# Kernel optimization log

Hardware: AMD Instinct MI355X
Metric: run time of the kernel (lower is better)

## Reference

```python
import jax, jax.numpy as jnp
import numpy as np

B, IN_DIM, H, OUT_DIM, T = 2048, 1024, 2048, 1024, 10


def setup_inputs() -> dict:
    key = jax.random.key(0)
    ks = jax.random.split(key, 16)
    s = lambda d: 1.0 / np.sqrt(d)
    inp = {
        "x": jax.random.normal(ks[0], (B, IN_DIM), jnp.float32),
        "z0": jax.random.normal(ks[1], (B, H), jnp.float32),
        "noise": jax.random.normal(ks[2], (T, B, H), jnp.float32),
        # input_embed: Linear(IN,H) -> SiLU -> Linear(H,H)
        "w1_in": jax.random.normal(ks[3], (IN_DIM, H), jnp.float32) * s(IN_DIM),
        "b1_in": jnp.zeros((H,), jnp.float32),
        "w2_in": jax.random.normal(ks[4], (H, H), jnp.float32) * s(H),
        "b2_in": jnp.zeros((H,), jnp.float32),
        # T blocks: Linear(2H,H) -> SiLU -> Linear(H,H), stacked over T
        "wA": jax.random.normal(ks[5], (T, 2 * H, H), jnp.float32) * s(2 * H),
        "bA": jnp.zeros((T, H), jnp.float32),
        "wB": jax.random.normal(ks[6], (T, H, H), jnp.float32) * s(H),
        "bB": jnp.zeros((T, H), jnp.float32),
        # classifier Linear(H, OUT)
        "wC": jax.random.normal(ks[7], (H, OUT_DIM), jnp.float32) * s(H),
        "bC": jnp.zeros((OUT_DIM,), jnp.float32),
    }
    return inp


def _forward(x, z0, noise, w1_in, b1_in, w2_in, b2_in, wA, bA, wB, bB, wC, bC):
    # input embedding
    h = jax.nn.silu(x @ w1_in + b1_in)
    x_embed = h @ w2_in + b2_in  # (B, H)

    alpha = jnp.linspace(0.99, 0.9, T).astype(x.dtype)          # (T,)
    noise_scale = jnp.sqrt(1.0 - alpha)                          # (T,)

    def step(z, per_t):
        wA_t, bA_t, wB_t, bB_t, n_t, a_t, ns_t = per_t
        u = jax.nn.silu(jnp.concatenate([z, x_embed], axis=-1) @ wA_t + bA_t)
        u = u @ wB_t + bB_t
        z_next = a_t * u + (1.0 - a_t) * z + ns_t * n_t
        return z_next, None

    z_final, _ = jax.lax.scan(step, z0, (wA, bA, wB, bB, noise, alpha, noise_scale))
    return z_final @ wC + bC  # (B, OUT_DIM)


def reference(x, z0, noise, w1_in, b1_in, w2_in, b2_in, wA, bA, wB, bB, wC, bC):
    return _forward(x, z0, noise, w1_in, b1_in, w2_in, b2_in, wA, bA, wB, bB, wC, bC)
```

## Files before the change

### kernel.cpp

```cpp
#include <hip/hip_runtime.h>
#include <math.h>

typedef _Float16 f16;
typedef _Float16 f16x4 __attribute__((ext_vector_type(4)));
typedef _Float16 f16x8 __attribute__((ext_vector_type(8)));
typedef float f32x4 __attribute__((ext_vector_type(4)));
typedef float fvec4 __attribute__((ext_vector_type(4)));

#define EP_SILU 0
#define EP_LIN  1
#define EP_ZUP  2
#define EP_OUT  3
#define EP_ADDP 4

struct TDesc {
  const float* W;
  f16* WT;
  long long sW, sWT;
  int R, C, nMat;
};

__device__ __forceinline__ void gll16(const void* g, void* l) {
  __builtin_amdgcn_global_load_lds((__attribute__((address_space(1))) void*)g,
                                   (__attribute__((address_space(3))) void*)l,
                                   16, 0, 0);
}

__device__ __forceinline__ void stage_tile(const f16* __restrict__ g, int ld,
                                           f16* ldsTile, int tid, int wid) {
#pragma unroll
  for (int p = 0; p < 2; ++p) {
    int row = p * 64 + (tid >> 2);
    int col = (tid & 3) * 8;
    gll16(g + (size_t)row * ld + col, ldsTile + p * 2048 + wid * 512);
  }
}

__device__ __forceinline__ void stage8s(const f16* __restrict__ g, int ld,
                                        f16* ldsTile, int tid) {
  int row = tid >> 2;
  int q = (tid & 3) ^ ((tid >> 3) & 3);
  gll16(g + (size_t)row * ld + q * 8, ldsTile + tid * 8);
}

__device__ __forceinline__ void tpose_tile(const float* __restrict__ W,
                                           f16* __restrict__ WT, int R, int C,
                                           int r0, int c0, f16 (*t)[72],
                                           int tid) {
#pragma unroll
  for (int p = 0; p < 2; ++p) {
    int lin = p * 2048 + tid * 4;
    int r = lin >> 6, c4 = lin & 63;
    fvec4 v = *(const fvec4*)(W + (size_t)(r0 + r) * C + c0 + c4);
    t[c4 + 0][r] = (f16)v[0];
    t[c4 + 1][r] = (f16)v[1];
    t[c4 + 2][r] = (f16)v[2];
    t[c4 + 3][r] = (f16)v[3];
  }
  __syncthreads();
#pragma unroll
  for (int p = 0; p < 2; ++p) {
    int lin = p * 2048 + tid * 4;
    int c = lin >> 6, r4 = lin & 63;
    f16x4 h;
    h[0] = t[c][r4 + 0];
    h[1] = t[c][r4 + 1];
    h[2] = t[c][r4 + 2];
    h[3] = t[c][r4 + 3];
    *(f16x4*)(WT + (size_t)(c0 + c) * R + r0 + r4) = h;
  }
  __syncthreads();
}

__device__ void run_role(const TDesc d, int rid, int nr, f16 (*t)[72],
                         int tid) {
  if (d.nMat <= 0 || d.W == nullptr) return;
  int tR = d.R >> 6, tC = d.C >> 6;
  int tpm = tR * tC, tot = tpm * d.nMat;
  for (int i = rid; i < tot; i += nr) {
    int m = i / tpm, rem = i - m * tpm;
    int r0 = (rem % tR) << 6, c0 = (rem / tR) << 6;
    tpose_tile(d.W + (size_t)m * d.sW, d.WT + (size_t)m * d.sWT, d.R, d.C, r0,
               c0, t, tid);
  }
}

#define GEMM8_ITER(KP, VM, DO_STAGE)                                          \
  {                                                                           \
    asm volatile("s_waitcnt vmcnt(" #VM ")" ::: "memory");                    \
    __builtin_amdgcn_s_barrier();                                             \
    const int slot_ = (KP) & 1;                                               \
    const f16* LA_ = base + slot_ * 16384 + h * 4096;                         \
    const f16* LB_ = base + slot_ * 16384 + 8192 + h * 4096;                  \
    f16x8 a_[4], b_[4];                                                       \
    _Pragma("unroll") for (int m_ = 0; m_ < 4; ++m_) a_[m_] =                 \
        *(const f16x8*)(LA_ +                                                 \
                        ((wr * 64 + m_ * 16 + lr) * 32 + (kg ^ xq) * 8));     \
    _Pragma("unroll") for (int n_ = 0; n_ < 4; ++n_) b_[n_] =                 \
        *(const f16x8*)(LB_ +                                                 \
                        ((wc * 64 + n_ * 16 + lr) * 32 + (kg ^ xq) * 8));     \
    asm volatile("s_waitcnt lgkmcnt(0)" ::: "memory");                        \
    __builtin_amdgcn_s_barrier();                                             \
    if (DO_STAGE) stageAB((KP) + 2, slot_);                                   \
    _Pragma("unroll") for (int m_ = 0; m_ < 4; ++m_)                          \
        _Pragma("unroll") for (int n_ = 0; n_ < 4; ++n_) acc[m_][n_] =        \
            __builtin_amdgcn_mfma_f32_16x16x32_f16(a_[m_], b_[n_],            \
                                                   acc[m_][n_], 0, 0, 0);     \
  }

template <int EP>
__global__ void __launch_bounds__(512)
gemm8(const f16* __restrict__ A, int lda, const f16* __restrict__ BT, int ldb,
      long long sBT, int K, int N, int gx, int nbGemm,
      const float* __restrict__ bias, long long sBias,
      const f16* __restrict__ addP, f16* __restrict__ outH,
      float* __restrict__ outF, long long sOut, const f16* __restrict__ zOld,
      const float* __restrict__ noise, float aT, float nsT, TDesc dA,
      TDesc dB) {
  __shared__ __align__(16) char smem[65536];
  const int tid = threadIdx.x;
  const int bid = blockIdx.x;

  if (bid >= nbGemm) {
    if (blockIdx.z == 0) {
      int rid = bid - nbGemm, nr = (int)gridDim.x - nbGemm;
      f16(*t)[72] = reinterpret_cast<f16(*)[72]>(smem);
      run_role(dA, rid, nr, t, tid);
      run_role(dB, rid, nr, t, tid);
    }
    return;
  }

  const int z = blockIdx.z;
  const f16* BTz = BT + (size_t)z * sBT;
  f16* outHz = outH ? outH + (size_t)z * sOut : nullptr;
  float* outFz = outF ? outF + (size_t)z * sOut : nullptr;

  const int cpx = nbGemm >> 3;
  const int swz = (bid & 7) * cpx + (bid >> 3);
  const int by = swz / gx, bx = swz % gx;
  const int m0 = by * 128, n0 = bx * 128;

  const int lane = tid & 63, wid = tid >> 6;
  const int q = wid & 3, h = wid >> 2;
  const int wr = q >> 1, wc = q & 1;
  const int lr = lane & 15, kg = lane >> 4;
  const int xq = (lr >> 1) & 3;

  f16* base = (f16*)smem;
  f32x4 acc[4][4] = {};

  const int nkp = K >> 6;
  auto stageAB = [&](int kp, int slot) {
    int k0 = kp << 6;
    f16* s = base + slot * 16384;
    stage8s(A + (size_t)m0 * lda + k0, lda, s, tid);
    stage8s(A + (size_t)m0 * lda + k0 + 32, lda, s + 4096, tid);
    stage8s(BTz + (size_t)n0 * ldb + k0, ldb, s + 8192, tid);
    stage8s(BTz + (size_t)n0 * ldb + k0 + 32, ldb, s + 12288, tid);
  };

  stageAB(0, 0);
  stageAB(1, 1);
  int kp = 0;
  for (; kp < nkp - 1; ++kp) GEMM8_ITER(kp, 4, (kp + 2 < nkp));
  GEMM8_ITER(kp, 0, 0);

  float* red = (float*)smem;
  if (h == 1) {
#pragma unroll
    for (int m = 0; m < 4; ++m)
#pragma unroll
      for (int n = 0; n < 4; ++n) {
        int row = wr * 64 + m * 16 + kg * 4;
        int col = wc * 64 + n * 16 + lr;
        int rs = row ^ ((col & 7) << 2);
        *(f32x4*)&red[(size_t)col * 128 + rs] = acc[m][n];
      }
  }
  __syncthreads();
  if (h != 0) return;

  float bcol[4];
  if constexpr (EP != EP_ADDP) {
    const float* biasz = bias + (size_t)z * sBias;
#pragma unroll
    for (int n = 0; n < 4; ++n) bcol[n] = biasz[n0 + wc * 64 + n * 16 + lr];
  }

#pragma unroll
  for (int m = 0; m < 4; ++m) {
    int rowb = m0 + wr * 64 + m * 16 + kg * 4;
    int rowl = wr * 64 + m * 16 + kg * 4;
#pragma unroll
    for (int n = 0; n < 4; ++n) {
      int col = n0 + wc * 64 + n * 16 + lr;
      int coll = wc * 64 + n * 16 + lr;
      int rsl = rowl ^ ((coll & 7) << 2);
      f32x4 osum = acc[m][n] + *(const f32x4*)&red[(size_t)coll * 128 + rsl];
#pragma unroll
      for (int r = 0; r < 4; ++r) {
        size_t idx = (size_t)(rowb + r) * N + col;
        float v = osum[r];
        if constexpr (EP == EP_ADDP) v += (float)addP[idx];
        else v += bcol[n];
        if constexpr (EP == EP_SILU || EP == EP_ADDP) {
          v = v / (1.0f + __expf(-v));
          outHz[idx] = (f16)v;
        } else if constexpr (EP == EP_LIN) {
          outHz[idx] = (f16)v;
        } else if constexpr (EP == EP_OUT) {
          outFz[idx] = v;
        } else {
          float zn = aT * v + (1.0f - aT) * (float)zOld[idx] + nsT * noise[idx];
          outHz[idx] = (f16)zn;
        }
      }
    }
  }
}

template <int EP>
__global__ void __launch_bounds__(256)
gemm_bt(const f16* __restrict__ A0, const f16* __restrict__ A1, int Ksplit,
        int lda, const f16* __restrict__ BT, int ldb, long long sBT, int K,
        int N, int gx, const float* __restrict__ bias, long long sBias,
        f16* __restrict__ outH, float* __restrict__ outF, long long sOut,
        const float* __restrict__ zOld, const float* __restrict__ noise,
        float aT, float nsT) {
  __shared__ __align__(16) f16 lds[2][2][128 * 32];
  const int tid = threadIdx.x;
  const int z = blockIdx.z;
  const f16* BTz = BT + (size_t)z * sBT;
  f16* outHz = outH ? outH + (size_t)z * sOut : nullptr;
  float* outFz = outF ? outF + (size_t)z * sOut : nullptr;

  const int lane = tid & 63, wid = tid >> 6;
  const int wr = wid >> 1, wc = wid & 1;
  const int lr = lane & 15, kg = lane >> 4;
  const int by = blockIdx.x / gx, bx = blockIdx.x - by * gx;
  const int m0 = by * 128, n0 = bx * 128;

  f32x4 acc[4][4] = {};
  const int nk = K >> 5;
  auto stageAB = [&](int kt, int buf) {
    int k0 = kt << 5;
    const f16* Abase = (k0 < Ksplit)
                           ? (A0 + (size_t)m0 * lda + k0)
                           : (A1 + (size_t)m0 * lda + (k0 - Ksplit));
    stage_tile(Abase, lda, &lds[buf][0][0], tid, wid);
    stage_tile(BTz + (size_t)n0 * ldb + k0, ldb, &lds[buf][1][0], tid, wid);
  };

  stageAB(0, 0);
  __syncthreads();
  int cur = 0;
  for (int kt = 0; kt < nk; ++kt) {
    if (kt + 1 < nk) stageAB(kt + 1, cur ^ 1);
    const f16* LA = &lds[cur][0][0];
    const f16* LB = &lds[cur][1][0];
    f16x8 a[4], b[4];
#pragma unroll
    for (int m = 0; m < 4; ++m)
      a[m] = *(const f16x8*)(LA + ((wr * 64 + m * 16 + lr) * 32 + kg * 8));
#pragma unroll
    for (int n = 0; n < 4; ++n)
      b[n] = *(const f16x8*)(LB + ((wc * 64 + n * 16 + lr) * 32 + kg * 8));
#pragma unroll
    for (int m = 0; m < 4; ++m)
#pragma unroll
      for (int n = 0; n < 4; ++n)
        acc[m][n] = __builtin_amdgcn_mfma_f32_16x16x32_f16(a[m], b[n],
                                                           acc[m][n], 0, 0, 0);
    __syncthreads();
    cur ^= 1;
  }

  float bcol[4];
  const float* biasz = bias + (size_t)z * sBias;
#pragma unroll
  for (int n = 0; n < 4; ++n) bcol[n] = biasz[n0 + wc * 64 + n * 16 + lr];

#pragma unroll
  for (int m = 0; m < 4; ++m) {
    int rowb = m0 + wr * 64 + m * 16 + kg * 4;
#pragma unroll
    for (int n = 0; n < 4; ++n) {
      int col = n0 + wc * 64 + n * 16 + lr;
#pragma unroll
      for (int r = 0; r < 4; ++r) {
        size_t idx = (size_t)(rowb + r) * N + col;
        float v = acc[m][n][r] + bcol[n];
        if constexpr (EP == EP_SILU) {
          v = v / (1.0f + __expf(-v));
          outHz[idx] = (f16)v;
        } else if constexpr (EP == EP_LIN) {
          outHz[idx] = (f16)v;
        } else if constexpr (EP == EP_OUT) {
          outFz[idx] = v;
        } else {
          float zn = aT * v + (1.0f - aT) * zOld[idx] + nsT * noise[idx];
          outFz[idx] = zn;
          outHz[idx] = (f16)zn;
        }
      }
    }
  }
}

__global__ void __launch_bounds__(512) tconv_role(TDesc d) {
  __shared__ __align__(16) f16 t[64][72];
  run_role(d, blockIdx.x, gridDim.x, t, threadIdx.x);
}

__global__ void __launch_bounds__(256)
cvt4(const float* __restrict__ in, f16* __restrict__ outp, int n4) {
  int i = blockIdx.x * 256 + threadIdx.x;
  if (i >= n4) return;
  fvec4 v = *(const fvec4*)(in + (size_t)i * 4);
  f16x4 h;
  h[0] = (f16)v[0];
  h[1] = (f16)v[1];
  h[2] = (f16)v[2];
  h[3] = (f16)v[3];
  *(f16x4*)(outp + (size_t)i * 4) = h;
}

__global__ void __launch_bounds__(256)
zinit4(const float* __restrict__ z0, float* __restrict__ z32,
       f16* __restrict__ z16, int n4) {
  int i = blockIdx.x * 256 + threadIdx.x;
  if (i >= n4) return;
  fvec4 v = *(const fvec4*)(z0 + (size_t)i * 4);
  *(fvec4*)(z32 + (size_t)i * 4) = v;
  f16x4 h;
  h[0] = (f16)v[0];
  h[1] = (f16)v[1];
  h[2] = (f16)v[2];
  h[3] = (f16)v[3];
  *(f16x4*)(z16 + (size_t)i * 4) = h;
}

extern "C" void kernel_launch(void* const* d_in, const int* in_sizes, int n_in,
                              void* d_out, int out_size, void* d_ws,
                              size_t ws_size, hipStream_t stream) {
  const int B = 2048, IN = 1024, H = 2048, OUT = 1024, T = 10;
  const float* x = (const float*)d_in[0];
  const float* z0 = (const float*)d_in[1];
  const float* noise = (const float*)d_in[2];
  const float* w1 = (const float*)d_in[3];
  const float* b1 = (const float*)d_in[4];
  const float* w2 = (const float*)d_in[5];
  const float* b2 = (const float*)d_in[6];
  const float* wA = (const float*)d_in[7];
  const float* bA = (const float*)d_in[8];
  const float* wB = (const float*)d_in[9];
  const float* bB = (const float*)d_in[10];
  const float* wC = (const float*)d_in[11];
  const float* bC = (const float*)d_in[12];
  float* out = (float*)d_out;

  char* ws = (char*)d_ws;
  size_t off = 0;
  auto alloc = [&](size_t bytes) {
    void* p = ws + off;
    off += (bytes + 255) & ~(size_t)255;
    return p;
  };
  TDesc none = {nullptr, nullptr, 0, 0, 0, 0, 0};

  const size_t FAST_NEED = 273000000ull;
  if (ws_size >= FAST_NEED) {
    f16* x16 = (f16*)alloc((size_t)B * IN * 2);
    f16* h16 = (f16*)alloc((size_t)B * H * 2);
    f16* xe16 = (f16*)alloc((size_t)B * H * 2);
    f16* z16 = (f16*)alloc((size_t)B * H * 2);
    f16* u16 = (f16*)alloc((size_t)B * H * 2);
    f16* p16 = (f16*)alloc((size_t)T * B * H * 2);
    f16* w1T = (f16*)alloc((size_t)IN * H * 2);
    f16* w2T = (f16*)alloc((size_t)H * H * 2);
    f16* wCT = (f16*)alloc((size_t)H * OUT * 2);
    f16* wAbotT = (f16*)alloc((size_t)T * H * H * 2);
    f16* wAtopT[2] = {(f16*)alloc((size_t)H * H * 2),
                      (f16*)alloc((size_t)H * H * 2)};
    f16* wBT2[2] = {(f16*)alloc((size_t)H * H * 2),
                    (f16*)alloc((size_t)H * H * 2)};

    cvt4<<<B * IN / 4 / 256, 256, 0, stream>>>(x, x16, B * IN / 4);
    cvt4<<<B * H / 4 / 256, 256, 0, stream>>>(z0, z16, B * H / 4);
    tconv_role<<<512, 512, 0, stream>>>(TDesc{w1, w1T, 0, 0, IN, H, 1});

    gemm8<EP_SILU><<<512, 512, 0, stream>>>(
        x16, IN, w1T, IN, 0, IN, H, 16, 256, b1, 0, nullptr, h16, nullptr, 0,
        nullptr, nullptr, 0.f, 0.f, TDesc{w2, w2T, 0, 0, H, H, 1},
        TDesc{wA + (size_t)H * H, wAbotT, (long long)2 * H * H,
              (long long)H * H, H, H, 4});
    gemm8<EP_LIN><<<512, 512, 0, stream>>>(
        h16, H, w2T, H, 0, H, H, 16, 256, b2, 0, nullptr, xe16, nullptr, 0,
        nullptr, nullptr, 0.f, 0.f, TDesc{wC, wCT, 0, 0, H, OUT, 1},
        TDesc{wA + (size_t)H * H + (size_t)4 * 2 * H * H,
              wAbotT + (size_t)4 * H * H, (long long)2 * H * H,
              (long long)H * H, H, H, 6});
    tconv_role<<<512, 512, 0, stream>>>(TDesc{wA, wAtopT[0], 0, 0, H, H, 1});

    gemm8<EP_LIN><<<dim3(256, 1, T), 512, 0, stream>>>(
        xe16, H, wAbotT, H, (long long)H * H, H, H, 16, 256, bA, H, nullptr,
        p16, nullptr, (long long)B * H, nullptr, nullptr, 0.f, 0.f, none,
        none);

    for (int t = 0; t < T; ++t) {
      float alpha = (float)(0.99 - 0.01 * (double)t);
      float ns = sqrtf(1.0f - alpha);
      gemm8<EP_ADDP><<<320, 512, 0, stream>>>(
          z16, H, wAtopT[t & 1], H, 0, H, H, 16, 256, nullptr, 0,
          p16 + (size_t)t * B * H, u16, nullptr, 0, nullptr, nullptr, 0.f,
          0.f, TDesc{wB + (size_t)t * H * H, wBT2[t & 1], 0, 0, H, H, 1},
          none);
      TDesc nextA = (t < T - 1)
                        ? TDesc{wA + (size_t)(t + 1) * 2 * H * H,
                                wAtopT[(t + 1) & 1], 0, 0, H, H, 1}
                        : none;
      gemm8<EP_ZUP><<<320, 512, 0, stream>>>(
          u16, H, wBT2[t & 1], H, 0, H, H, 16, 256, bB + (size_t)t * H, 0,
          nullptr, z16, nullptr, 0, z16, noise + (size_t)t * B * H, alpha, ns,
          nextA, none);
    }
    gemm8<EP_OUT><<<128, 512, 0, stream>>>(
        z16, H, wCT, H, 0, H, OUT, 8, 128, bC, 0, nullptr, nullptr, out, 0,
        nullptr, nullptr, 0.f, 0.f, none, none);
  } else {
    f16* x16 = (f16*)alloc((size_t)B * IN * 2);
    f16* h16 = (f16*)alloc((size_t)B * H * 2);
    f16* xe16 = (f16*)alloc((size_t)B * H * 2);
    f16* z16 = (f16*)alloc((size_t)B * H * 2);
    f16* u16 = (f16*)alloc((size_t)B * H * 2);
    float* z32 = (float*)alloc((size_t)B * H * 4);
    f16* w1T = (f16*)alloc((size_t)IN * H * 2);
    f16* w2T = (f16*)alloc((size_t)H * H * 2);
    f16* wCT = (f16*)alloc((size_t)H * OUT * 2);
    f16* wAT = (f16*)alloc((size_t)2 * H * H * 2);
    f16* wBT = (f16*)alloc((size_t)H * H * 2);

    cvt4<<<B * IN / 4 / 256, 256, 0, stream>>>(x, x16, B * IN / 4);
    zinit4<<<B * H / 4 / 256, 256, 0, stream>>>(z0, z32, z16, B * H / 4);
    tconv_role<<<512, 512, 0, stream>>>(TDesc{w1, w1T, 0, 0, IN, H, 1});
    tconv_role<<<1024, 512, 0, stream>>>(TDesc{w2, w2T, 0, 0, H, H, 1});
    tconv_role<<<512, 512, 0, stream>>>(TDesc{wC, wCT, 0, 0, H, OUT, 1});

    gemm_bt<EP_SILU><<<dim3(256, 1, 1), 256, 0, stream>>>(
        x16, x16, IN, IN, w1T, IN, 0, IN, H, 16, b1, 0, h16, nullptr, 0,
        nullptr, nullptr, 0.f, 0.f);
    gemm_bt<EP_LIN><<<dim3(256, 1, 1), 256, 0, stream>>>(
        h16, h16, H, H, w2T, H, 0, H, H, 16, b2, 0, xe16, nullptr, 0, nullptr,
        nullptr, 0.f, 0.f);

    for (int t = 0; t < T; ++t) {
      float alpha = (float)(0.99 - 0.01 * (double)t);
      float ns = sqrtf(1.0f - alpha);
      tconv_role<<<1024, 512, 0, stream>>>(
          TDesc{wA + (size_t)t * 2 * H * H, wAT, 0, 0, 2 * H, H, 1});
      gemm_bt<EP_SILU><<<dim3(256, 1, 1), 256, 0, stream>>>(
          z16, xe16, H, H, wAT, 2 * H, 0, 2 * H, H, 16, bA + (size_t)t * H, 0,
          u16, nullptr, 0, nullptr, nullptr, 0.f, 0.f);
      tconv_role<<<1024, 512, 0, stream>>>(
          TDesc{wB + (size_t)t * H * H, wBT, 0, 0, H, H, 1});
      gemm_bt<EP_ZUP><<<dim3(256, 1, 1), 256, 0, stream>>>(
          u16, u16, H, H, wBT, H, 0, H, H, 16, bB + (size_t)t * H, 0, z16,
          z32, 0, z32, noise + (size_t)t * B * H, alpha, ns);
    }
    gemm_bt<EP_OUT><<<dim3(128, 1, 1), 256, 0, stream>>>(
        z16, z16, H, H, wCT, H, 0, H, OUT, 8, bC, 0, nullptr, out, 0, nullptr,
        nullptr, 0.f, 0.f);
  }
}
```

Baseline: 1.109 ms.

## Fuse recurrent timestep loop into one persistent kernel with per-panel barriers

Replaces the 20 per-timestep GEMM launches and the final classifier launch with one persistent 256-block kernel. Each group of 16 blocks owns one 128-row panel of z and syncs through atomic-counter barriers instead of kernel boundaries. All wA-top and wB transposes now run up front, as extra blocks of the batched p-projection GEMM. This removes launch gaps and tail effects, at the cost of more workspace, spin-wait barriers and a dependence on all 256 blocks being resident at once.

```diff
diff --git a/kernel.cpp b/kernel.cpp
--- a/kernel.cpp
+++ b/kernel.cpp
@@ -109,18 +109,98 @@
   }
 
 template <int EP>
+__device__ __forceinline__ void
+gphase(const f16* __restrict__ A, int lda, const f16* __restrict__ BT,
+       int ldb, int K, int N, int m0, int n0, const float* __restrict__ bias,
+       const f16* __restrict__ addP, f16* __restrict__ outH,
+       float* __restrict__ outF, const f16* __restrict__ zOld,
+       const float* __restrict__ noise, float aT, float nsT, f16* base,
+       int tid) {
+  const int lane = tid & 63, wid = tid >> 6;
+  const int q = wid & 3, h = wid >> 2;
+  const int wr = q >> 1, wc = q & 1;
+  const int lr = lane & 15, kg = lane >> 4;
+  const int xq = (lr >> 1) & 3;
+
+  f32x4 acc[4][4] = {};
+  const int nkp = K >> 6;
+  auto stageAB = [&](int kp, int slot) {
+    int k0 = kp << 6;
+    f16* s = base + slot * 16384;
+    stage8s(A + (size_t)m0 * lda + k0, lda, s, tid);
+    stage8s(A + (size_t)m0 * lda + k0 + 32, lda, s + 4096, tid);
+    stage8s(BT + (size_t)n0 * ldb + k0, ldb, s + 8192, tid);
+    stage8s(BT + (size_t)n0 * ldb + k0 + 32, ldb, s + 12288, tid);
+  };
+
+  stageAB(0, 0);
+  stageAB(1, 1);
+  int kp = 0;
+  for (; kp < nkp - 1; ++kp) GEMM8_ITER(kp, 4, (kp + 2 < nkp));
+  GEMM8_ITER(kp, 0, 0);
+
+  float* red = (float*)base;
+  if (h == 1) {
+#pragma unroll
+    for (int m = 0; m < 4; ++m)
+#pragma unroll
+      for (int n = 0; n < 4; ++n) {
+        int row = wr * 64 + m * 16 + kg * 4;
+        int col = wc * 64 + n * 16 + lr;
+        int rs = row ^ ((col & 7) << 2);
+        *(f32x4*)&red[(size_t)col * 128 + rs] = acc[m][n];
+      }
+  }
+  __syncthreads();
+  if (h == 0) {
+    float bcol[4];
+    if constexpr (EP != EP_ADDP) {
+#pragma unroll
+      for (int n = 0; n < 4; ++n) bcol[n] = bias[n0 + wc * 64 + n * 16 + lr];
+    }
+#pragma unroll
+    for (int m = 0; m < 4; ++m) {
+      int rowb = m0 + wr * 64 + m * 16 + kg * 4;
+      int rowl = wr * 64 + m * 16 + kg * 4;
+#pragma unroll
+      for (int n = 0; n < 4; ++n) {
+        int col = n0 + wc * 64 + n * 16 + lr;
+        int coll = wc * 64 + n * 16 + lr;
+        int rsl = rowl ^ ((coll & 7) << 2);
+        f32x4 osum =
+            acc[m][n] + *(const f32x4*)&red[(size_t)coll * 128 + rsl];
+#pragma unroll
+        for (int r = 0; r < 4; ++r) {
+          size_t idx = (size_t)(rowb + r) * N + col;
+          float v = osum[r];
+          if constexpr (EP == EP_ADDP) v += (float)addP[idx];
+          else v += bcol[n];
+          if constexpr (EP == EP_SILU || EP == EP_ADDP) {
+            v = v / (1.0f + __expf(-v));
+            outH[idx] = (f16)v;
+          } else if constexpr (EP == EP_LIN) {
+            outH[idx] = (f16)v;
+          } else if constexpr (EP == EP_OUT) {
+            outF[idx] = v;
+          } else {
+            float zn =
+                aT * v + (1.0f - aT) * (float)zOld[idx] + nsT * noise[idx];
+            outH[idx] = (f16)zn;
+          }
+        }
+      }
+    }
+  }
+}
+
+template <int EP>
 __global__ void __launch_bounds__(512)
 gemm8(const f16* __restrict__ A, int lda, const f16* __restrict__ BT, int ldb,
       long long sBT, int K, int N, int gx, int nbGemm,
-      const float* __restrict__ bias, long long sBias,
-      const f16* __restrict__ addP, f16* __restrict__ outH,
-      float* __restrict__ outF, long long sOut, const f16* __restrict__ zOld,
-      const float* __restrict__ noise, float aT, float nsT, TDesc dA,
-      TDesc dB) {
+      const float* __restrict__ bias, long long sBias, f16* __restrict__ outH,
+      long long sOut, TDesc dA, TDesc dB) {
   __shared__ __align__(16) char smem[65536];
-  const int tid = threadIdx.x;
-  const int bid = blockIdx.x;
-
+  const int tid = threadIdx.x, bid = blockIdx.x;
   if (bid >= nbGemm) {
     if (blockIdx.z == 0) {
       int rid = bid - nbGemm, nr = (int)gridDim.x - nbGemm;
@@ -130,94 +210,62 @@
     }
     return;
   }
-
   const int z = blockIdx.z;
-  const f16* BTz = BT + (size_t)z * sBT;
-  f16* outHz = outH ? outH + (size_t)z * sOut : nullptr;
-  float* outFz = outF ? outF + (size_t)z * sOut : nullptr;
-
   const int cpx = nbGemm >> 3;
   const int swz = (bid & 7) * cpx + (bid >> 3);
   const int by = swz / gx, bx = swz % gx;
-  const int m0 = by * 128, n0 = bx * 128;
-
-  const int lane = tid & 63, wid = tid >> 6;
-  const int q = wid & 3, h = wid >> 2;
-  const int wr = q >> 1, wc = q & 1;
-  const int lr = lane & 15, kg = lane >> 4;
-  const int xq = (lr >> 1) & 3;
-
+  gphase<EP>(A, lda, BT + (size_t)z * sBT, ldb, K, N, by * 128, bx * 128,
+             bias + (size_t)z * sBias, nullptr, outH + (size_t)z * sOut,
+             nullptr, nullptr, nullptr, 0.f, 0.f, (f16*)smem, tid);
+}
+
+__device__ __forceinline__ void panelbar(unsigned* cnt, unsigned target,
+                                         int tid) {
+  __syncthreads();
+  if (tid == 0) {
+    __threadfence();
+    atomicAdd(cnt, 1u);
+    while (atomicAdd(cnt, 0u) < target) __builtin_amdgcn_s_sleep(2);
+    __threadfence();
+  }
+  __syncthreads();
+}
+
+__global__ void __launch_bounds__(512)
+fused_loop(f16* __restrict__ z16, f16* __restrict__ u16,
+           const f16* __restrict__ p16, const f16* __restrict__ wAtopT,
+           const f16* __restrict__ wBT, const float* __restrict__ bB,
+           const float* __restrict__ noise, const f16* __restrict__ wCT,
+           const float* __restrict__ bC, float* __restrict__ out,
+           unsigned* __restrict__ bar) {
+  constexpr int H = 2048, Bv = 2048, T = 10, OUTD = 1024;
+  __shared__ __align__(16) char smem[65536];
   f16* base = (f16*)smem;
-  f32x4 acc[4][4] = {};
-
-  const int nkp = K >> 6;
-  auto stageAB = [&](int kp, int slot) {
-    int k0 = kp << 6;
-    f16* s = base + slot * 16384;
-    stage8s(A + (size_t)m0 * lda + k0, lda, s, tid);
-    stage8s(A + (size_t)m0 * lda + k0 + 32, lda, s + 4096, tid);
-    stage8s(BTz + (size_t)n0 * ldb + k0, ldb, s + 8192, tid);
-    stage8s(BTz + (size_t)n0 * ldb + k0 + 32, ldb, s + 12288, tid);
-  };
-
-  stageAB(0, 0);
-  stageAB(1, 1);
-  int kp = 0;
-  for (; kp < nkp - 1; ++kp) GEMM8_ITER(kp, 4, (kp + 2 < nkp));
-  GEMM8_ITER(kp, 0, 0);
-
-  float* red = (float*)smem;
-  if (h == 1) {
-#pragma unroll
-    for (int m = 0; m < 4; ++m)
-#pragma unroll
-      for (int n = 0; n < 4; ++n) {
-        int row = wr * 64 + m * 16 + kg * 4;
-        int col = wc * 64 + n * 16 + lr;
-        int rs = row ^ ((col & 7) << 2);
-        *(f32x4*)&red[(size_t)col * 128 + rs] = acc[m][n];
-      }
-  }
-  __syncthreads();
-  if (h != 0) return;
-
-  float bcol[4];
-  if constexpr (EP != EP_ADDP) {
-    const float* biasz = bias + (size_t)z * sBias;
-#pragma unroll
-    for (int n = 0; n < 4; ++n) bcol[n] = biasz[n0 + wc * 64 + n * 16 + lr];
-  }
-
-#pragma unroll
-  for (int m = 0; m < 4; ++m) {
-    int rowb = m0 + wr * 64 + m * 16 + kg * 4;
-    int rowl = wr * 64 + m * 16 + kg * 4;
-#pragma unroll
-    for (int n = 0; n < 4; ++n) {
-      int col = n0 + wc * 64 + n * 16 + lr;
-      int coll = wc * 64 + n * 16 + lr;
-      int rsl = rowl ^ ((coll & 7) << 2);
-      f32x4 osum = acc[m][n] + *(const f32x4*)&red[(size_t)coll * 128 + rsl];
-#pragma unroll
-      for (int r = 0; r < 4; ++r) {
-        size_t idx = (size_t)(rowb + r) * N + col;
-        float v = osum[r];
-        if constexpr (EP == EP_ADDP) v += (float)addP[idx];
-        else v += bcol[n];
-        if constexpr (EP == EP_SILU || EP == EP_ADDP) {
-          v = v / (1.0f + __expf(-v));
-          outHz[idx] = (f16)v;
-        } else if constexpr (EP == EP_LIN) {
-          outHz[idx] = (f16)v;
-        } else if constexpr (EP == EP_OUT) {
-          outFz[idx] = v;
-        } else {
-          float zn = aT * v + (1.0f - aT) * (float)zOld[idx] + nsT * noise[idx];
-          outHz[idx] = (f16)zn;
-        }
-      }
-    }
-  }
+  const int tid = threadIdx.x, bid = blockIdx.x;
+  const int s = bid >> 3;
+  const int ch = (bid & 7) + 8 * (s >> 4);
+  const int bx = s & 15;
+  const int m0 = ch * 128;
+  unsigned gen = 0;
+  unsigned* cnt = bar + ch * 32;
+
+  for (int t = 0; t < T; ++t) {
+    float alpha = (float)(0.99 - 0.01 * (double)t);
+    float ns = sqrtf(1.0f - alpha);
+    gphase<EP_ADDP>(z16, H, wAtopT + (size_t)t * H * H, H, H, H, m0, bx * 128,
+                    nullptr, p16 + (size_t)t * Bv * H, u16, nullptr, nullptr,
+                    nullptr, 0.f, 0.f, base, tid);
+    ++gen;
+    panelbar(cnt, 16u * gen, tid);
+    gphase<EP_ZUP>(u16, H, wBT + (size_t)t * H * H, H, H, H, m0, bx * 128,
+                   bB + (size_t)t * H, nullptr, z16, nullptr, z16,
+                   noise + (size_t)t * Bv * H, alpha, ns, base, tid);
+    ++gen;
+    panelbar(cnt, 16u * gen, tid);
+  }
+  if (bx < 8)
+    gphase<EP_OUT>(z16, H, wCT, H, H, OUTD, m0, bx * 128, bC, nullptr,
+                   nullptr, out, nullptr, nullptr, 0.f, 0.f, base, tid);
 }
 
 template <int EP>
@@ -369,8 +417,9 @@
   };
   TDesc none = {nullptr, nullptr, 0, 0, 0, 0, 0};
 
-  const size_t FAST_NEED = 273000000ull;
+  const size_t FAST_NEED = 380000000ull;
   if (ws_size >= FAST_NEED) {
+    unsigned* bar = (unsigned*)alloc(2048);
     f16* x16 = (f16*)alloc((size_t)B * IN * 2);
     f16* h16 = (f16*)alloc((size_t)B * H * 2);
     f16* xe16 = (f16*)alloc((size_t)B * H * 2);
@@ -381,53 +430,34 @@
     f16* w2T = (f16*)alloc((size_t)H * H * 2);
     f16* wCT = (f16*)alloc((size_t)H * OUT * 2);
     f16* wAbotT = (f16*)alloc((size_t)T * H * H * 2);
-    f16* wAtopT[2] = {(f16*)alloc((size_t)H * H * 2),
-                      (f16*)alloc((size_t)H * H * 2)};
-    f16* wBT2[2] = {(f16*)alloc((size_t)H * H * 2),
-                    (f16*)alloc((size_t)H * H * 2)};
-
+    f16* wAtopT = (f16*)alloc((size_t)T * H * H * 2);
+    f16* wBTall = (f16*)alloc((size_t)T * H * H * 2);
+
+    hipMemsetAsync(bar, 0, 2048, stream);
     cvt4<<<B * IN / 4 / 256, 256, 0, stream>>>(x, x16, B * IN / 4);
     cvt4<<<B * H / 4 / 256, 256, 0, stream>>>(z0, z16, B * H / 4);
     tconv_role<<<512, 512, 0, stream>>>(TDesc{w1, w1T, 0, 0, IN, H, 1});
 
     gemm8<EP_SILU><<<512, 512, 0, stream>>>(
-        x16, IN, w1T, IN, 0, IN, H, 16, 256, b1, 0, nullptr, h16, nullptr, 0,
-        nullptr, nullptr, 0.f, 0.f, TDesc{w2, w2T, 0, 0, H, H, 1},
+        x16, IN, w1T, IN, 0, IN, H, 16, 256, b1, 0, h16, 0,
+        TDesc{w2, w2T, 0, 0, H, H, 1},
         TDesc{wA + (size_t)H * H, wAbotT, (long long)2 * H * H,
-              (long long)H * H, H, H, 4});
+              (long long)H * H, H, H, 5});
     gemm8<EP_LIN><<<512, 512, 0, stream>>>(
-        h16, H, w2T, H, 0, H, H, 16, 256, b2, 0, nullptr, xe16, nullptr, 0,
-        nullptr, nullptr, 0.f, 0.f, TDesc{wC, wCT, 0, 0, H, OUT, 1},
-        TDesc{wA + (size_t)H * H + (size_t)4 * 2 * H * H,
-              wAbotT + (size_t)4 * H * H, (long long)2 * H * H,
-              (long long)H * H, H, H, 6});
-    tconv_role<<<512, 512, 0, stream>>>(TDesc{wA, wAtopT[0], 0, 0, H, H, 1});
-
-    gemm8<EP_LIN><<<dim3(256, 1, T), 512, 0, stream>>>(
-        xe16, H, wAbotT, H, (long long)H * H, H, H, 16, 256, bA, H, nullptr,
-        p16, nullptr, (long long)B * H, nullptr, nullptr, 0.f, 0.f, none,
-        none);
-
-    for (int t = 0; t < T; ++t) {
-      float alpha = (float)(0.99 - 0.01 * (double)t);
-      float ns = sqrtf(1.0f - alpha);
-      gemm8<EP_ADDP><<<320, 512, 0, stream>>>(
-          z16, H, wAtopT[t & 1], H, 0, H, H, 16, 256, nullptr, 0,
-          p16 + (size_t)t * B * H, u16, nullptr, 0, nullptr, nullptr, 0.f,
-          0.f, TDesc{wB + (size_t)t * H * H, wBT2[t & 1], 0, 0, H, H, 1},
-          none);
-      TDesc nextA = (t < T - 1)
-                        ? TDesc{wA + (size_t)(t + 1) * 2 * H * H,
-                                wAtopT[(t + 1) & 1], 0, 0, H, H, 1}
-                        : none;
-      gemm8<EP_ZUP><<<320, 512, 0, stream>>>(
-          u16, H, wBT2[t & 1], H, 0, H, H, 16, 256, bB + (size_t)t * H, 0,
-          nullptr, z16, nullptr, 0, z16, noise + (size_t)t * B * H, alpha, ns,
-          nextA, none);
-    }
-    gemm8<EP_OUT><<<128, 512, 0, stream>>>(
-        z16, H, wCT, H, 0, H, OUT, 8, 128, bC, 0, nullptr, nullptr, out, 0,
-        nullptr, nullptr, 0.f, 0.f, none, none);
+        h16, H, w2T, H, 0, H, H, 16, 256, b2, 0, xe16, 0,
+        TDesc{wC, wCT, 0, 0, H, OUT, 1},
+        TDesc{wA + (size_t)H * H + (size_t)5 * 2 * H * H,
+              wAbotT + (size_t)5 * H * H, (long long)2 * H * H,
+              (long long)H * H, H, H, 5});
+
+    gemm8<EP_LIN><<<dim3(384, 1, T), 512, 0, stream>>>(
+        xe16, H, wAbotT, H, (long long)H * H, H, H, 16, 256, bA, H, p16,
+        (long long)B * H,
+        TDesc{wA, wAtopT, (long long)2 * H * H, (long long)H * H, H, H, 10},
+        TDesc{wB, wBTall, (long long)H * H, (long long)H * H, H, H, 10});
+
+    fused_loop<<<256, 512, 0, stream>>>(z16, u16, p16, wAtopT, wBTall, bB,
+                                        noise, wCT, bC, out, bar);
   } else {
     f16* x16 = (f16*)alloc((size_t)B * IN * 2);
     f16* h16 = (f16*)alloc((size_t)B * H * 2);
```

After: 1.554 ms. +40.2%, slower.

## Double-buffer LDS fragments in registers to overlap loads with MFMAs

Applied to the files above, without the earlier changes.

Replaces the GEMM main-loop macro with a software-pipelined loop. Each iteration now loads the next k-step's A/B fragments from LDS into a second register set while the MFMAs for the current step run, with a sched_barrier keeping the compiler from reordering them. This is meant to hide LDS read latency behind matrix math and drops the second barrier per iteration. In exchange it uses more VGPRs and waits with vmcnt(0) every iteration, so global prefetch only runs one step ahead instead of two.

```diff
diff --git a/kernel.cpp b/kernel.cpp
--- a/kernel.cpp
+++ b/kernel.cpp
@@ -84,29 +84,6 @@
                c0, t, tid);
   }
 }
-
-#define GEMM8_ITER(KP, VM, DO_STAGE)                                          \
-  {                                                                           \
-    asm volatile("s_waitcnt vmcnt(" #VM ")" ::: "memory");                    \
-    __builtin_amdgcn_s_barrier();                                             \
-    const int slot_ = (KP) & 1;                                               \
-    const f16* LA_ = base + slot_ * 16384 + h * 4096;                         \
-    const f16* LB_ = base + slot_ * 16384 + 8192 + h * 4096;                  \
-    f16x8 a_[4], b_[4];                                                       \
-    _Pragma("unroll") for (int m_ = 0; m_ < 4; ++m_) a_[m_] =                 \
-        *(const f16x8*)(LA_ +                                                 \
-                        ((wr * 64 + m_ * 16 + lr) * 32 + (kg ^ xq) * 8));     \
-    _Pragma("unroll") for (int n_ = 0; n_ < 4; ++n_) b_[n_] =                 \
-        *(const f16x8*)(LB_ +                                                 \
-                        ((wc * 64 + n_ * 16 + lr) * 32 + (kg ^ xq) * 8));     \
-    asm volatile("s_waitcnt lgkmcnt(0)" ::: "memory");                        \
-    __builtin_amdgcn_s_barrier();                                             \
-    if (DO_STAGE) stageAB((KP) + 2, slot_);                                   \
-    _Pragma("unroll") for (int m_ = 0; m_ < 4; ++m_)                          \
-        _Pragma("unroll") for (int n_ = 0; n_ < 4; ++n_) acc[m_][n_] =        \
-            __builtin_amdgcn_mfma_f32_16x16x32_f16(a_[m_], b_[n_],            \
-                                                   acc[m_][n_], 0, 0, 0);     \
-  }
 
 template <int EP>
 __global__ void __launch_bounds__(512)
@@ -159,12 +136,48 @@
     stage8s(BTz + (size_t)n0 * ldb + k0, ldb, s + 8192, tid);
     stage8s(BTz + (size_t)n0 * ldb + k0 + 32, ldb, s + 12288, tid);
   };
+  auto LDF = [&](f16x8* aa, f16x8* bb, int kp) {
+    const int slot_ = kp & 1;
+    const f16* LA_ = base + slot_ * 16384 + h * 4096;
+    const f16* LB_ = base + slot_ * 16384 + 8192 + h * 4096;
+#pragma unroll
+    for (int m_ = 0; m_ < 4; ++m_)
+      aa[m_] = *(const f16x8*)(LA_ +
+                               ((wr * 64 + m_ * 16 + lr) * 32 + (kg ^ xq) * 8));
+#pragma unroll
+    for (int n_ = 0; n_ < 4; ++n_)
+      bb[n_] = *(const f16x8*)(LB_ +
+                               ((wc * 64 + n_ * 16 + lr) * 32 + (kg ^ xq) * 8));
+  };
 
   stageAB(0, 0);
   stageAB(1, 1);
-  int kp = 0;
-  for (; kp < nkp - 1; ++kp) GEMM8_ITER(kp, 4, (kp + 2 < nkp));
-  GEMM8_ITER(kp, 0, 0);
+  asm volatile("s_waitcnt vmcnt(4)" ::: "memory");
+  __builtin_amdgcn_s_barrier();
+  f16x8 a[4], b[4], a2[4], b2[4];
+  LDF(a, b, 0);
+  asm volatile("s_waitcnt lgkmcnt(0)" ::: "memory");
+
+  for (int kp = 0; kp < nkp; ++kp) {
+    asm volatile("s_waitcnt vmcnt(0)" ::: "memory");
+    __builtin_amdgcn_s_barrier();
+    if (kp + 2 < nkp) stageAB(kp + 2, kp & 1);
+    if (kp + 1 < nkp) LDF(a2, b2, kp + 1);
+    __builtin_amdgcn_sched_barrier(0);
+#pragma unroll
+    for (int m_ = 0; m_ < 4; ++m_)
+#pragma unroll
+      for (int n_ = 0; n_ < 4; ++n_)
+        acc[m_][n_] = __builtin_amdgcn_mfma_f32_16x16x32_f16(a[m_], b[n_],
+                                                             acc[m_][n_], 0,
+                                                             0, 0);
+    asm volatile("s_waitcnt lgkmcnt(0)" ::: "memory");
+#pragma unroll
+    for (int i_ = 0; i_ < 4; ++i_) {
+      a[i_] = a2[i_];
+      b[i_] = b2[i_];
+    }
+  }
 
   float* red = (float*)smem;
   if (h == 1) {
```

Result: slower. 1.374 ms (+24.0%).

## Replace split-K 512-thread GEMM with per-wave private-tile 256-thread GEMM

Applied to the files above, without the earlier changes.

Adds a new gemmw kernel in which each of four waves owns its own 64x64 output tile and stages its own A/B slices into private LDS double buffers. This removes block-wide barriers and the cross-half split-K reduction through LDS. The recurrent step GEMMs, the embedding GEMMs and the classifier now use gemmw, and the transpose role moves to 256 threads. gemm8 is kept only for the batched precompute, at the cost of no A/B data sharing between waves.

```diff
diff --git a/kernel.cpp b/kernel.cpp
--- a/kernel.cpp
+++ b/kernel.cpp
@@ -48,8 +48,8 @@
                                            int r0, int c0, f16 (*t)[72],
                                            int tid) {
 #pragma unroll
-  for (int p = 0; p < 2; ++p) {
-    int lin = p * 2048 + tid * 4;
+  for (int p = 0; p < 4; ++p) {
+    int lin = p * 1024 + tid * 4;
     int r = lin >> 6, c4 = lin & 63;
     fvec4 v = *(const fvec4*)(W + (size_t)(r0 + r) * C + c0 + c4);
     t[c4 + 0][r] = (f16)v[0];
@@ -59,8 +59,8 @@
   }
   __syncthreads();
 #pragma unroll
-  for (int p = 0; p < 2; ++p) {
-    int lin = p * 2048 + tid * 4;
+  for (int p = 0; p < 4; ++p) {
+    int lin = p * 1024 + tid * 4;
     int c = lin >> 6, r4 = lin & 63;
     f16x4 h;
     h[0] = t[c][r4 + 0];
@@ -82,6 +82,117 @@
     int r0 = (rem % tR) << 6, c0 = (rem / tR) << 6;
     tpose_tile(d.W + (size_t)m * d.sW, d.WT + (size_t)m * d.sWT, d.R, d.C, r0,
                c0, t, tid);
+  }
+}
+
+template <int EP>
+__global__ void __launch_bounds__(256, 1)
+gemmw(const f16* __restrict__ A, int lda, const f16* __restrict__ BT, int ldb,
+      int K, int N, int gx, int nbGemm, const float* __restrict__ bias,
+      const f16* __restrict__ addP, f16* __restrict__ outH,
+      float* __restrict__ outF, const f16* __restrict__ zOld,
+      const float* __restrict__ noise, float aT, float nsT, TDesc dA,
+      TDesc dB) {
+  __shared__ __align__(16) f16 lds[32768];
+  const int tid = threadIdx.x, bid = blockIdx.x;
+
+  if (bid >= nbGemm) {
+    int rid = bid - nbGemm, nr = (int)gridDim.x - nbGemm;
+    f16(*t)[72] = reinterpret_cast<f16(*)[72]>(lds);
+    run_role(dA, rid, nr, t, tid);
+    run_role(dB, rid, nr, t, tid);
+    return;
+  }
+
+  const int cpx = nbGemm >> 3;
+  const int swz = (bid & 7) * cpx + (bid >> 3);
+  const int by = swz / gx, bx = swz % gx;
+
+  const int lane = tid & 63, wid = tid >> 6;
+  const int tm0 = by * 128 + (wid >> 1) * 64;
+  const int tn0 = bx * 128 + (wid & 1) * 64;
+  const int lr = lane & 15, kg = lane >> 4;
+  const int xq = (lr >> 1) & 3;
+  f16* wbase = lds + wid * 8192;
+
+  f32x4 acc[4][4] = {};
+  const int nk = K >> 5;
+
+  auto stageW = [&](int kp, int slot) {
+    int k0 = kp << 5;
+    f16* s = wbase + slot * 4096;
+#pragma unroll
+    for (int i = 0; i < 4; ++i) {
+      int pos = i * 64 + lane;
+      int row = pos >> 2;
+      int q = (pos & 3) ^ ((pos >> 3) & 3);
+      gll16(A + (size_t)(tm0 + row) * lda + k0 + q * 8, s + pos * 8);
+    }
+#pragma unroll
+    for (int i = 0; i < 4; ++i) {
+      int pos = i * 64 + lane;
+      int row = pos >> 2;
+      int q = (pos & 3) ^ ((pos >> 3) & 3);
+      gll16(BT + (size_t)(tn0 + row) * ldb + k0 + q * 8, s + 2048 + pos * 8);
+    }
+  };
+
+  stageW(0, 0);
+  stageW(1, 1);
+  for (int kp = 0; kp < nk; ++kp) {
+    if (kp < nk - 1)
+      asm volatile("s_waitcnt vmcnt(8)" ::: "memory");
+    else
+      asm volatile("s_waitcnt vmcnt(0)" ::: "memory");
+    const f16* sa = wbase + (kp & 1) * 4096;
+    const f16* sb = sa + 2048;
+    f16x8 a[4], b[4];
+#pragma unroll
+    for (int m = 0; m < 4; ++m)
+      a[m] = *(const f16x8*)(sa + (m * 16 + lr) * 32 + (kg ^ xq) * 8);
+#pragma unroll
+    for (int n = 0; n < 4; ++n)
+      b[n] = *(const f16x8*)(sb + (n * 16 + lr) * 32 + (kg ^ xq) * 8);
+    asm volatile("s_waitcnt lgkmcnt(0)" ::: "memory");
+    if (kp + 2 < nk) stageW(kp + 2, kp & 1);
+#pragma unroll
+    for (int m = 0; m < 4; ++m)
+#pragma unroll
+      for (int n = 0; n < 4; ++n)
+        acc[m][n] = __builtin_amdgcn_mfma_f32_16x16x32_f16(a[m], b[n],
+                                                           acc[m][n], 0, 0, 0);
+  }
+
+  float bcol[4];
+  if constexpr (EP != EP_ADDP) {
+#pragma unroll
+    for (int n = 0; n < 4; ++n) bcol[n] = bias[tn0 + n * 16 + lr];
+  }
+#pragma unroll
+  for (int m = 0; m < 4; ++m) {
+    int rowb = tm0 + m * 16 + kg * 4;
+#pragma unroll
+    for (int n = 0; n < 4; ++n) {
+      int col = tn0 + n * 16 + lr;
+#pragma unroll
+      for (int r = 0; r < 4; ++r) {
+        size_t idx = (size_t)(rowb + r) * N + col;
+        float v = acc[m][n][r];
+        if constexpr (EP == EP_ADDP) v += (float)addP[idx];
+        else v += bcol[n];
+        if constexpr (EP == EP_SILU || EP == EP_ADDP) {
+          v = v / (1.0f + __expf(-v));
+          outH[idx] = (f16)v;
+        } else if constexpr (EP == EP_LIN) {
+          outH[idx] = (f16)v;
+        } else if constexpr (EP == EP_OUT) {
+          outF[idx] = v;
+        } else {
+          float zn = aT * v + (1.0f - aT) * (float)zOld[idx] + nsT * noise[idx];
+          outH[idx] = (f16)zn;
+        }
+      }
+    }
   }
 }
 
@@ -112,29 +223,13 @@
 __global__ void __launch_bounds__(512)
 gemm8(const f16* __restrict__ A, int lda, const f16* __restrict__ BT, int ldb,
       long long sBT, int K, int N, int gx, int nbGemm,
-      const float* __restrict__ bias, long long sBias,
-      const f16* __restrict__ addP, f16* __restrict__ outH,
-      float* __restrict__ outF, long long sOut, const f16* __restrict__ zOld,
-      const float* __restrict__ noise, float aT, float nsT, TDesc dA,
-      TDesc dB) {
+      const float* __restrict__ bias, long long sBias, f16* __restrict__ outH,
+      long long sOut) {
   __shared__ __align__(16) char smem[65536];
-  const int tid = threadIdx.x;
-  const int bid = blockIdx.x;
-
-  if (bid >= nbGemm) {
-    if (blockIdx.z == 0) {
-      int rid = bid - nbGemm, nr = (int)gridDim.x - nbGemm;
-      f16(*t)[72] = reinterpret_cast<f16(*)[72]>(smem);
-      run_role(dA, rid, nr, t, tid);
-      run_role(dB, rid, nr, t, tid);
-    }
-    return;
-  }
-
+  const int tid = threadIdx.x, bid = blockIdx.x;
   const int z = blockIdx.z;
   const f16* BTz = BT + (size_t)z * sBT;
-  f16* outHz = outH ? outH + (size_t)z * sOut : nullptr;
-  float* outFz = outF ? outF + (size_t)z * sOut : nullptr;
+  f16* outHz = outH + (size_t)z * sOut;
 
   const int cpx = nbGemm >> 3;
   const int swz = (bid & 7) * cpx + (bid >> 3);
@@ -182,11 +277,9 @@
   if (h != 0) return;
 
   float bcol[4];
-  if constexpr (EP != EP_ADDP) {
-    const float* biasz = bias + (size_t)z * sBias;
-#pragma unroll
-    for (int n = 0; n < 4; ++n) bcol[n] = biasz[n0 + wc * 64 + n * 16 + lr];
-  }
+  const float* biasz = bias + (size_t)z * sBias;
+#pragma unroll
+  for (int n = 0; n < 4; ++n) bcol[n] = biasz[n0 + wc * 64 + n * 16 + lr];
 
 #pragma unroll
   for (int m = 0; m < 4; ++m) {
@@ -201,20 +294,7 @@
 #pragma unroll
       for (int r = 0; r < 4; ++r) {
         size_t idx = (size_t)(rowb + r) * N + col;
-        float v = osum[r];
-        if constexpr (EP == EP_ADDP) v += (float)addP[idx];
-        else v += bcol[n];
-        if constexpr (EP == EP_SILU || EP == EP_ADDP) {
-          v = v / (1.0f + __expf(-v));
-          outHz[idx] = (f16)v;
-        } else if constexpr (EP == EP_LIN) {
-          outHz[idx] = (f16)v;
-        } else if constexpr (EP == EP_OUT) {
-          outFz[idx] = v;
-        } else {
-          float zn = aT * v + (1.0f - aT) * (float)zOld[idx] + nsT * noise[idx];
-          outHz[idx] = (f16)zn;
-        }
+        outHz[idx] = (f16)(osum[r] + bcol[n]);
       }
     }
   }
@@ -308,7 +388,7 @@
   }
 }
 
-__global__ void __launch_bounds__(512) tconv_role(TDesc d) {
+__global__ void __launch_bounds__(256) tconv_role(TDesc d) {
   __shared__ __align__(16) f16 t[64][72];
   run_role(d, blockIdx.x, gridDim.x, t, threadIdx.x);
 }
@@ -388,46 +468,44 @@
 
     cvt4<<<B * IN / 4 / 256, 256, 0, stream>>>(x, x16, B * IN / 4);
     cvt4<<<B * H / 4 / 256, 256, 0, stream>>>(z0, z16, B * H / 4);
-    tconv_role<<<512, 512, 0, stream>>>(TDesc{w1, w1T, 0, 0, IN, H, 1});
-
-    gemm8<EP_SILU><<<512, 512, 0, stream>>>(
-        x16, IN, w1T, IN, 0, IN, H, 16, 256, b1, 0, nullptr, h16, nullptr, 0,
-        nullptr, nullptr, 0.f, 0.f, TDesc{w2, w2T, 0, 0, H, H, 1},
+    tconv_role<<<512, 256, 0, stream>>>(TDesc{w1, w1T, 0, 0, IN, H, 1});
+
+    gemmw<EP_SILU><<<320, 256, 0, stream>>>(
+        x16, IN, w1T, IN, IN, H, 16, 256, b1, nullptr, h16, nullptr, nullptr,
+        nullptr, 0.f, 0.f, TDesc{w2, w2T, 0, 0, H, H, 1},
         TDesc{wA + (size_t)H * H, wAbotT, (long long)2 * H * H,
               (long long)H * H, H, H, 4});
-    gemm8<EP_LIN><<<512, 512, 0, stream>>>(
-        h16, H, w2T, H, 0, H, H, 16, 256, b2, 0, nullptr, xe16, nullptr, 0,
-        nullptr, nullptr, 0.f, 0.f, TDesc{wC, wCT, 0, 0, H, OUT, 1},
+    gemmw<EP_LIN><<<320, 256, 0, stream>>>(
+        h16, H, w2T, H, H, H, 16, 256, b2, nullptr, xe16, nullptr, nullptr,
+        nullptr, 0.f, 0.f, TDesc{wC, wCT, 0, 0, H, OUT, 1},
         TDesc{wA + (size_t)H * H + (size_t)4 * 2 * H * H,
               wAbotT + (size_t)4 * H * H, (long long)2 * H * H,
               (long long)H * H, H, H, 6});
-    tconv_role<<<512, 512, 0, stream>>>(TDesc{wA, wAtopT[0], 0, 0, H, H, 1});
+    tconv_role<<<256, 256, 0, stream>>>(TDesc{wA, wAtopT[0], 0, 0, H, H, 1});
 
     gemm8<EP_LIN><<<dim3(256, 1, T), 512, 0, stream>>>(
-        xe16, H, wAbotT, H, (long long)H * H, H, H, 16, 256, bA, H, nullptr,
-        p16, nullptr, (long long)B * H, nullptr, nullptr, 0.f, 0.f, none,
-        none);
+        xe16, H, wAbotT, H, (long long)H * H, H, H, 16, 256, bA, H, p16,
+        (long long)B * H);
 
     for (int t = 0; t < T; ++t) {
       float alpha = (float)(0.99 - 0.01 * (double)t);
       float ns = sqrtf(1.0f - alpha);
-      gemm8<EP_ADDP><<<320, 512, 0, stream>>>(
-          z16, H, wAtopT[t & 1], H, 0, H, H, 16, 256, nullptr, 0,
-          p16 + (size_t)t * B * H, u16, nullptr, 0, nullptr, nullptr, 0.f,
-          0.f, TDesc{wB + (size_t)t * H * H, wBT2[t & 1], 0, 0, H, H, 1},
-          none);
+      gemmw<EP_ADDP><<<320, 256, 0, stream>>>(
+          z16, H, wAtopT[t & 1], H, H, H, 16, 256, nullptr,
+          p16 + (size_t)t * B * H, u16, nullptr, nullptr, nullptr, 0.f, 0.f,
+          TDesc{wB + (size_t)t * H * H, wBT2[t & 1], 0, 0, H, H, 1}, none);
       TDesc nextA = (t < T - 1)
                         ? TDesc{wA + (size_t)(t + 1) * 2 * H * H,
                                 wAtopT[(t + 1) & 1], 0, 0, H, H, 1}
                         : none;
-      gemm8<EP_ZUP><<<320, 512, 0, stream>>>(
-          u16, H, wBT2[t & 1], H, 0, H, H, 16, 256, bB + (size_t)t * H, 0,
-          nullptr, z16, nullptr, 0, z16, noise + (size_t)t * B * H, alpha, ns,
-          nextA, none);
-    }
-    gemm8<EP_OUT><<<128, 512, 0, stream>>>(
-        z16, H, wCT, H, 0, H, OUT, 8, 128, bC, 0, nullptr, nullptr, out, 0,
-        nullptr, nullptr, 0.f, 0.f, none, none);
+      gemmw<EP_ZUP><<<320, 256, 0, stream>>>(
+          u16, H, wBT2[t & 1], H, H, H, 16, 256, bB + (size_t)t * H, nullptr,
+          z16, nullptr, z16, noise + (size_t)t * B * H, alpha, ns, nextA,
+          none);
+    }
+    gemmw<EP_OUT><<<128, 256, 0, stream>>>(
+        z16, H, wCT, H, H, OUT, 8, 128, bC, nullptr, nullptr, out, nullptr,
+        nullptr, 0.f, 0.f, none, none);
   } else {
     f16* x16 = (f16*)alloc((size_t)B * IN * 2);
     f16* h16 = (f16*)alloc((size_t)B * H * 2);
@@ -443,9 +521,9 @@
 
     cvt4<<<B * IN / 4 / 256, 256, 0, stream>>>(x, x16, B * IN / 4);
     zinit4<<<B * H / 4 / 256, 256, 0, stream>>>(z0, z32, z16, B * H / 4);
-    tconv_role<<<512, 512, 0, stream>>>(TDesc{w1, w1T, 0, 0, IN, H, 1});
-    tconv_role<<<1024, 512, 0, stream>>>(TDesc{w2, w2T, 0, 0, H, H, 1});
-    tconv_role<<<512, 512, 0, stream>>>(TDesc{wC, wCT, 0, 0, H, OUT, 1});
+    tconv_role<<<512, 256, 0, stream>>>(TDesc{w1, w1T, 0, 0, IN, H, 1});
+    tconv_role<<<1024, 256, 0, stream>>>(TDesc{w2, w2T, 0, 0, H, H, 1});
+    tconv_role<<<512, 256, 0, stream>>>(TDesc{wC, wCT, 0, 0, H, OUT, 1});
 
     gemm_bt<EP_SILU><<<dim3(256, 1, 1), 256, 0, stream>>>(
         x16, x16, IN, IN, w1T, IN, 0, IN, H, 16, b1, 0, h16, nullptr, 0,
@@ -457,12 +535,12 @@
     for (int t = 0; t < T; ++t) {
       float alpha = (float)(0.99 - 0.01 * (double)t);
       float ns = sqrtf(1.0f - alpha);
-      tconv_role<<<1024, 512, 0, stream>>>(
+      tconv_role<<<1024, 256, 0, stream>>>(
           TDesc{wA + (size_t)t * 2 * H * H, wAT, 0, 0, 2 * H, H, 1});
       gemm_bt<EP_SILU><<<dim3(256, 1, 1), 256, 0, stream>>>(
           z16, xe16, H, H, wAT, 2 * H, 0, 2 * H, H, 16, bA + (size_t)t * H, 0,
           u16, nullptr, 0, nullptr, nullptr, 0.f, 0.f);
-      tconv_role<<<1024, 512, 0, stream>>>(
+      tconv_role<<<1024, 256, 0, stream>>>(
           TDesc{wB + (size_t)t * H * H, wBT, 0, 0, H, H, 1});
       gemm_bt<EP_ZUP><<<dim3(256, 1, 1), 256, 0, stream>>>(
           u16, u16, H, H, wBT, H, 0, H, H, 16, bB + (size_t)t * H, 0, z16,
```

Result: slower. 1.431 ms (+29.0%).
